# Kernel tuning notes

Hardware: AMD Instinct MI355X
Metric: run time of the kernel (lower is better)

## Reference

```python
import jax, jax.numpy as jnp
import numpy as np

N = 50000      # nodes
E = 640000     # edges
F_IN = 64      # node feature dim
H = 128        # hidden channels
G = 256        # graphs in batch
NEG_SLOPE = 0.2
BN_EPS = 1e-5


def setup_inputs() -> dict:
    key = jax.random.key(0)
    ks = jax.random.split(key, 32)
    rn = lambda k, shape, s=0.1: jax.random.normal(k, shape, dtype=jnp.float32) * s
    inp = {
        'x': jax.random.normal(ks[0], (N, F_IN), dtype=jnp.float32),
        'edge_index': jax.random.randint(ks[1], (2, E), 0, N, dtype=jnp.int32),
        'batch': jnp.sort(jax.random.randint(ks[2], (N,), 0, G, dtype=jnp.int32)),
        # GATConv 1
        'W1': rn(ks[3], (F_IN, H)), 'as1': rn(ks[4], (H,)), 'ad1': rn(ks[5], (H,)), 'b1': jnp.zeros((H,), jnp.float32),
        # GATConv 2
        'W2': rn(ks[6], (H, H)), 'as2': rn(ks[7], (H,)), 'ad2': rn(ks[8], (H,)), 'b2': jnp.zeros((H,), jnp.float32),
        # GATConv 3
        'W3': rn(ks[9], (H, H)), 'as3': rn(ks[10], (H,)), 'ad3': rn(ks[11], (H,)), 'b3': jnp.zeros((H,), jnp.float32),
        # BatchNorm (inference: running stats)
        'g1': jnp.ones((H,), jnp.float32), 'be1': jnp.zeros((H,), jnp.float32), 'm1': rn(ks[12], (H,), 0.01), 'v1': jnp.ones((H,), jnp.float32),
        'g2': jnp.ones((H,), jnp.float32), 'be2': jnp.zeros((H,), jnp.float32), 'm2': rn(ks[13], (H,), 0.01), 'v2': jnp.ones((H,), jnp.float32),
        'g3': jnp.ones((H,), jnp.float32), 'be3': jnp.zeros((H,), jnp.float32), 'm3': rn(ks[14], (H,), 0.01), 'v3': jnp.ones((H,), jnp.float32),
        # MLP head
        'lw1': rn(ks[15], (H, H)), 'lb1': jnp.zeros((H,), jnp.float32),
        'lw2': rn(ks[16], (H, 1)), 'lb2': jnp.zeros((1,), jnp.float32),
    }
    return inp


def gat_layer(x, src, dst, W, a_src, a_dst, b, n):
    # PyG GATConv, heads=1: linear, per-edge attention, segment softmax over dst, scatter-add.
    h = x @ W                                  # [N, H]
    s_src = h @ a_src                          # [N]
    s_dst = h @ a_dst                          # [N]
    e = jax.nn.leaky_relu(s_src[src] + s_dst[dst], NEG_SLOPE)   # [E']
    m = jax.ops.segment_max(e, dst, num_segments=n)
    ex = jnp.exp(e - m[dst])
    denom = jax.ops.segment_sum(ex, dst, num_segments=n)
    coef = ex / denom[dst]                     # softmax per destination node
    out = jax.ops.segment_sum(coef[:, None] * h[src], dst, num_segments=n)
    return out + b


def batch_norm(x, g, b, mean, var):
    return (x - mean) * jax.lax.rsqrt(var + BN_EPS) * g + b


def reference(x, edge_index, batch,
              W1, as1, ad1, b1, W2, as2, ad2, b2, W3, as3, ad3, b3,
              g1, be1, m1, v1, g2, be2, m2, v2, g3, be3, m3, v3,
              lw1, lb1, lw2, lb2):
    n = x.shape[0]
    loops = jnp.arange(n, dtype=edge_index.dtype)      # PyG adds self-loops by default
    src = jnp.concatenate([edge_index[0], loops])
    dst = jnp.concatenate([edge_index[1], loops])

    h = gat_layer(x, src, dst, W1, as1, ad1, b1, n)
    h = jax.nn.relu(batch_norm(h, g1, be1, m1, v1))
    h = gat_layer(h, src, dst, W2, as2, ad2, b2, n)
    h = jax.nn.relu(batch_norm(h, g2, be2, m2, v2))
    h = gat_layer(h, src, dst, W3, as3, ad3, b3, n)
    h = jax.nn.relu(batch_norm(h, g3, be3, m3, v3))

    # global_mean_pool
    counts = jax.ops.segment_sum(jnp.ones((n,), h.dtype), batch, num_segments=G)
    pooled = jax.ops.segment_sum(h, batch, num_segments=G) / jnp.maximum(counts, 1.0)[:, None]

    out = jax.nn.relu(pooled @ lw1 + lb1)
    out = out @ lw2 + lb2                               # [G, 1]
    return out
```

## Files before the change

### kernel.cpp

```cpp
#include <hip/hip_runtime.h>

#define HD 128
#define NEG 0.2f
#define BNEPS 1e-5f

typedef unsigned int uint32;
typedef __attribute__((ext_vector_type(8))) short short8;
typedef __attribute__((ext_vector_type(4))) float floatx4;


__device__ inline float wave_sum_f(float v) {
#pragma unroll
  for (int off = 32; off; off >>= 1) v += __shfl_xor(v, off, 64);
  return v;
}
__device__ inline int wave_iscan_i(int v, int lane) {
#pragma unroll
  for (int off = 1; off < 64; off <<= 1) {
    int t = __shfl_up(v, off, 64);
    if (lane >= off) v += t;
  }
  return v;
}
__device__ inline uint32 f2bf(float f) {
  uint32 u = __float_as_uint(f);
  return (u + 0x7fffu + ((u >> 16) & 1u)) >> 16;
}
__device__ inline void kpair(int kc, int lg, int e2, bool perm, int& k_lo, int& k_hi) {
  if (!perm) {
    k_lo = kc * 32 + lg * 8 + e2 * 2;
    k_hi = k_lo + 1;
  } else {
    int w = kc * 16 + lg * 4 + e2;
    k_lo = ((w >> 4) << 5) + (w & 15);
    k_hi = k_lo + 16;
  }
}

__global__ __launch_bounds__(256)
void k_pack(const float* __restrict__ W1, const float* __restrict__ as1v,
            const float* __restrict__ ad1v, const float* __restrict__ W2,
            const float* __restrict__ as2v, const float* __restrict__ ad2v,
            const float* __restrict__ W3, const float* __restrict__ as3v,
            const float* __restrict__ ad3v,
            const float* __restrict__ b1, const float* __restrict__ g1,
            const float* __restrict__ be1, const float* __restrict__ m1,
            const float* __restrict__ v1,
            const float* __restrict__ b2, const float* __restrict__ g2,
            const float* __restrict__ be2, const float* __restrict__ m2,
            const float* __restrict__ v2,
            const float* __restrict__ b3, const float* __restrict__ g3,
            const float* __restrict__ be3, const float* __restrict__ m3,
            const float* __restrict__ v3,
            uint32* __restrict__ PW1, uint32* __restrict__ PW2,
            uint32* __restrict__ PW3, uint32* __restrict__ BFA1,
            uint32* __restrict__ BFA2, uint32* __restrict__ BFA3,
            float4* __restrict__ BNAB, int* __restrict__ deg,
            int* __restrict__ gcnt, float* __restrict__ pooled, int G, int n) {
  const int b = blockIdx.x, t = threadIdx.x;
  if (b >= 83) {
    const int i = (b - 83) * 256 + t;
    if (i < n) deg[i] = 0;
    else if (i < n + G * HD) pooled[i - n] = 0.f;
    if (b == 83 && t == 0) gcnt[0] = 0;
    return;
  }
  if (b < 80) {
    const float* W;
    uint32* PW;
    int KC, local;
    bool perm;
    if (b < 16) { W = W1; PW = PW1; KC = 2; perm = false; local = b; }
    else if (b < 48) { W = W2; PW = PW2; KC = 4; perm = true; local = b - 16; }
    else { W = W3; PW = PW3; KC = 4; perm = true; local = b - 48; }
    const int idx = local * 256 + t;
    const int e2 = idx & 3, l = (idx >> 2) & 63, f = idx >> 8;
    const int kc = f % KC, ct = f / KC;
    int k_lo, k_hi;
    kpair(kc, l >> 4, e2, perm, k_lo, k_hi);
    const int col = ct * 16 + (l & 15);
    PW[idx] = f2bf(W[k_lo * HD + col]) | (f2bf(W[k_hi * HD + col]) << 16);
  } else {
    const int layer = b - 80;
    const float* W = layer == 0 ? W1 : layer == 1 ? W2 : W3;
    const float* av = layer == 0 ? as1v : layer == 1 ? as2v : as3v;
    const float* dv = layer == 0 ? ad1v : layer == 1 ? ad2v : ad3v;
    const float* bb = layer == 0 ? b1 : layer == 1 ? b2 : b3;
    const float* gg = layer == 0 ? g1 : layer == 1 ? g2 : g3;
    const float* bt = layer == 0 ? be1 : layer == 1 ? be2 : be3;
    const float* mm = layer == 0 ? m1 : layer == 1 ? m2 : m3;
    const float* vv = layer == 0 ? v1 : layer == 1 ? v2 : v3;
    uint32* BFA = layer == 0 ? BFA1 : layer == 1 ? BFA2 : BFA3;
    const int K = layer == 0 ? 64 : 128, KC = K / 32;
    const bool perm = layer != 0;
    __shared__ float ws[128], wd[128];
    if (t < K) {
      float s = 0.f, d = 0.f;
      for (int j = 0; j < HD; ++j) {
        const float w = W[t * HD + j];
        s = fmaf(w, av[j], s);
        d = fmaf(w, dv[j], d);
      }
      ws[t] = s;
      wd[t] = d;
    }
    __syncthreads();
    const int total = KC * 256;
    for (int idx = t; idx < total; idx += 256) {
      const int e2 = idx & 3, l = (idx >> 2) & 63, kc = idx >> 8;
      int k_lo, k_hi;
      kpair(kc, l >> 4, e2, perm, k_lo, k_hi);
      const int li = l & 15;
      const float lo = li == 0 ? ws[k_lo] : li == 1 ? wd[k_lo] : 0.f;
      const float hi = li == 0 ? ws[k_hi] : li == 1 ? wd[k_hi] : 0.f;
      BFA[idx] = f2bf(lo) | (f2bf(hi) << 16);
    }
    if (t < 64) {
      const int c0 = (t >> 4) * 32 + (t & 15);
      const int c1 = c0 + 16;
      const float A0 = gg[c0] * rsqrtf(vv[c0] + BNEPS);
      const float A1 = gg[c1] * rsqrtf(vv[c1] + BNEPS);
      float4 r;
      r.x = A0;
      r.y = (bb[c0] - mm[c0]) * A0 + bt[c0];
      r.z = A1;
      r.w = (bb[c1] - mm[c1]) * A1 + bt[c1];
      BNAB[layer * 64 + t] = r;
    }
  }
}

__global__ __launch_bounds__(256)
void k_alloc(const int* __restrict__ deg, int* __restrict__ gcnt,
             int2* __restrict__ offs2, int* __restrict__ csr,
             int* __restrict__ cursor, int n) {
  const int t = threadIdx.x, lane = t & 63, wave = t >> 6;
  const int i = blockIdx.x * 256 + t;
  const int v = (i < n) ? deg[i] + 1 : 0;
  const int x = wave_iscan_i(v, lane);
  __shared__ int wsum[4];
  __shared__ int bbase;
  if (lane == 63) wsum[wave] = x;
  __syncthreads();
  if (t == 0) bbase = atomicAdd(gcnt, wsum[0] + wsum[1] + wsum[2] + wsum[3]);
  __syncthreads();
  int add = bbase;
#pragma unroll
  for (int w = 0; w < 4; ++w)
    if (w < wave) add += wsum[w];
  const int start = add + x - v;
  if (i < n) {
    csr[start] = i;
    cursor[i] = start + 1;
    offs2[i] = make_int2(start, start + v);
  }
}

__global__ void k_fill_edges(const int* __restrict__ src, const int* __restrict__ dst,
                             int* __restrict__ cursor, int* __restrict__ csr, int E) {
  int i = blockIdx.x * blockDim.x + threadIdx.x;
  if (i < E) { int p = atomicAdd(&cursor[dst[i]], 1); csr[p] = src[i]; }
}

template <int K, bool BF16IN>
__device__ inline void gemm_body(int bid, const void* __restrict__ Xv,
                                 const uint32* __restrict__ PW,
                                 const uint32* __restrict__ BFA,
                                 uint32* __restrict__ Hh, float* __restrict__ ssrc,
                                 float* __restrict__ sdst, int n) {
  constexpr int KC = K / 32;
  __shared__ uint32 Xl[64 * K / 2];
  const int t = threadIdx.x;
  const int wv = t >> 6, l = t & 63;
  const int rowbase = bid * 64;

  short8 bfr[2][KC];
#pragma unroll
  for (int c2 = 0; c2 < 2; ++c2)
#pragma unroll
    for (int kc = 0; kc < KC; ++kc)
      bfr[c2][kc] = *((const short8*)PW + ((wv * 2 + c2) * KC + kc) * 64 + l);
  short8 bfa[KC];
  if (wv == 0) {
#pragma unroll
    for (int kc = 0; kc < KC; ++kc) bfa[kc] = *((const short8*)BFA + kc * 64 + l);
  }

  if (BF16IN) {
    const uint32* Xb = (const uint32*)Xv;
#pragma unroll
    for (int B = t; B < 64 * (K / 8); B += 256) {
      const int row = B / (K / 8), cb = B % (K / 8);
      const int r = min(rowbase + row, n - 1);
      const uint4 v = *(const uint4*)&Xb[(long)r * (K / 2) + cb * 4];
      *(uint4*)&Xl[row * (K / 2) + (cb ^ (row & 7)) * 4] = v;
    }
  } else {
    const float* X = (const float*)Xv;
    for (int i = t; i < 64 * (K / 4); i += 256) {
      const int row = i / (K / 4), kq = i % (K / 4);
      const int r = min(rowbase + row, n - 1);
      const float4 v = *(const float4*)&X[(long)r * K + kq * 4];
      uint2 p;
      p.x = f2bf(v.x) | (f2bf(v.y) << 16);
      p.y = f2bf(v.z) | (f2bf(v.w) << 16);
      int byte = row * (K * 2) + kq * 8;
      byte ^= (row & 7) << 4;
      *(uint2*)((char*)Xl + byte) = p;
    }
  }
  __syncthreads();

  floatx4 acc[4][2], acc2[4];
#pragma unroll
  for (int rt = 0; rt < 4; ++rt) {
    acc[rt][0] = (floatx4){0.f, 0.f, 0.f, 0.f};
    acc[rt][1] = (floatx4){0.f, 0.f, 0.f, 0.f};
    acc2[rt] = (floatx4){0.f, 0.f, 0.f, 0.f};
  }
  const int row_l = l & 15, kgrp = l >> 4;
#pragma unroll
  for (int rt = 0; rt < 4; ++rt) {
    const int row = rt * 16 + row_l;
#pragma unroll
    for (int kc = 0; kc < KC; ++kc) {
      const int byte = (row * (K * 2) + kc * 64 + kgrp * 16) ^ ((row & 7) << 4);
      const short8 af = *(const short8*)((const char*)Xl + byte);
      acc[rt][0] = __builtin_amdgcn_mfma_f32_16x16x32_bf16(af, bfr[0][kc], acc[rt][0], 0, 0, 0);
      acc[rt][1] = __builtin_amdgcn_mfma_f32_16x16x32_bf16(af, bfr[1][kc], acc[rt][1], 0, 0, 0);
      if (wv == 0)
        acc2[rt] = __builtin_amdgcn_mfma_f32_16x16x32_bf16(af, bfa[kc], acc2[rt], 0, 0, 0);
    }
  }

#pragma unroll
  for (int rt = 0; rt < 4; ++rt) {
#pragma unroll
    for (int r = 0; r < 4; ++r) {
      const int R = rowbase + rt * 16 + kgrp * 4 + r;
      if (R < n)
        Hh[(long)R * 64 + wv * 16 + row_l] =
            f2bf(acc[rt][0][r]) | (f2bf(acc[rt][1][r]) << 16);
    }
  }
  if (wv == 0 && row_l < 2) {
    float* tgt = (row_l == 0) ? ssrc : sdst;
#pragma unroll
    for (int rt = 0; rt < 4; ++rt)
#pragma unroll
      for (int r = 0; r < 4; ++r) {
        const int R = rowbase + rt * 16 + kgrp * 4 + r;
        if (R < n) tgt[R] = acc2[rt][r];
      }
  }
}

__global__ __launch_bounds__(256)
void k_gemm1_hist(const void* __restrict__ Xv, const uint32* __restrict__ PW,
                  const uint32* __restrict__ BFA, uint32* __restrict__ Hh,
                  float* __restrict__ ssrc, float* __restrict__ sdst, int n,
                  const int* __restrict__ dst, int* __restrict__ deg, int E, int GB) {
  const int b = blockIdx.x;
  if (b < GB) {
    gemm_body<64, false>(b, Xv, PW, BFA, Hh, ssrc, sdst, n);
  } else {
    const int i = (b - GB) * 256 + threadIdx.x;
    if (i < E) atomicAdd(&deg[dst[i]], 1);
  }
}

template <int K>
__global__ __launch_bounds__(256)
void k_gemm_mfma(const void* __restrict__ Xv, const uint32* __restrict__ PW,
                 const uint32* __restrict__ BFA, uint32* __restrict__ Hh,
                 float* __restrict__ ssrc, float* __restrict__ sdst, int n) {
  gemm_body<K, true>(blockIdx.x, Xv, PW, BFA, Hh, ssrc, sdst, n);
}

__global__ __launch_bounds__(256)
void k_agg(const uint32* __restrict__ Hh, const float* __restrict__ ssrc,
           const float* __restrict__ sdst, const int2* __restrict__ offs2,
           const int* __restrict__ csr, const float4* __restrict__ BNAB,
           uint32* __restrict__ Ybf, int n) {
  const int wid = (blockIdx.x * blockDim.x + threadIdx.x) >> 6;
  const int lane = threadIdx.x & 63;
  if (wid >= n) return;
  const int2 se = offs2[wid];
  const float sdv = sdst[wid];
  float acc0 = 0.f, acc1 = 0.f, denom = 0.f;
  for (int base = se.x; base < se.y; base += 64) {
    const int m = min(64, se.y - base);
    int sidx = 0;
    float p = 0.f;
    if (lane < m) {
      sidx = csr[base + lane];
      const float tt = ssrc[sidx] + sdv;
      const float e = (tt > 0.f) ? tt : NEG * tt;
      p = __expf(e);
    }
    denom += wave_sum_f(p);
    const uint32 pu = __float_as_uint(p);
    for (int jj = 0; jj < m; jj += 16) {
      uint32 g[16];
#pragma unroll
      for (int u = 0; u < 16; ++u) {
        if (jj + u < m) {
          const int s = __builtin_amdgcn_readlane(sidx, jj + u);
          g[u] = Hh[(long)s * 64 + lane];
        }
      }
#pragma unroll
      for (int u = 0; u < 16; ++u) {
        if (jj + u < m) {
          const float w = __uint_as_float(__builtin_amdgcn_readlane(pu, jj + u));
          acc0 = fmaf(w, __uint_as_float(g[u] << 16), acc0);
          acc1 = fmaf(w, __uint_as_float(g[u] & 0xffff0000u), acc1);
        }
      }
    }
  }
  const float inv = 1.f / denom;
  const float4 ab = BNAB[lane];
  const float v0 = fmaxf(fmaf(acc0 * inv, ab.x, ab.y), 0.f);
  const float v1 = fmaxf(fmaf(acc1 * inv, ab.z, ab.w), 0.f);
  Ybf[(long)wid * 64 + lane] = f2bf(v0) | (f2bf(v1) << 16);
}

__global__ __launch_bounds__(256)
void k_pool_part(const uint32* __restrict__ Ybf, const int* __restrict__ batch,
                 int n, float* __restrict__ pooled) {
  const int g = blockIdx.x >> 2, q = blockIdx.x & 3;
  const int wave = threadIdx.x >> 6, lane = threadIdx.x & 63;
  int lo = 0, hi = n;
  while (lo < hi) { int mid = (lo + hi) >> 1; if (batch[mid] < g) lo = mid + 1; else hi = mid; }
  const int start = lo;
  hi = n;
  while (lo < hi) { int mid = (lo + hi) >> 1; if (batch[mid] < g + 1) lo = mid + 1; else hi = mid; }
  const int len = lo - start;
  const int qs = start + (len * q) / 4;
  const int qe = start + (len * (q + 1)) / 4;
  const int c0 = (lane >> 4) * 32 + (lane & 15), c1 = c0 + 16;
  float m0 = 0.f, m1 = 0.f;
  for (int i = qs + wave; i < qe; i += 4) {
    const uint32 gv = Ybf[(long)i * 64 + lane];
    m0 += __uint_as_float(gv << 16);
    m1 += __uint_as_float(gv & 0xffff0000u);
  }
  __shared__ float red[4][HD];
  red[wave][c0] = m0;
  red[wave][c1] = m1;
  __syncthreads();
  if (wave == 0) {
    m0 = red[0][c0] + red[1][c0] + red[2][c0] + red[3][c0];
    m1 = red[0][c1] + red[1][c1] + red[2][c1] + red[3][c1];
    atomicAdd(&pooled[g * HD + c0], m0);
    atomicAdd(&pooled[g * HD + c1], m1);
  }
}

__global__ __launch_bounds__(256)
void k_head(const float* __restrict__ pooled, const int* __restrict__ batch, int n,
            int G, const float* __restrict__ lw1, const float* __restrict__ lb1,
            const float* __restrict__ lw2, const float* __restrict__ lb2,
            float* __restrict__ out) {
  const int g = blockIdx.x * 4 + (threadIdx.x >> 6);
  const int lane = threadIdx.x & 63;
  if (g >= G) return;
  int lo = 0, hi = n;
  while (lo < hi) { int mid = (lo + hi) >> 1; if (batch[mid] < g) lo = mid + 1; else hi = mid; }
  const int start = lo;
  hi = n;
  while (lo < hi) { int mid = (lo + hi) >> 1; if (batch[mid] < g + 1) lo = mid + 1; else hi = mid; }
  const int cnt = lo - start;
  const float invc = (cnt > 0) ? 1.f / (float)cnt : 0.f;
  const int c0 = (lane >> 4) * 32 + (lane & 15), c1 = c0 + 16;
  const float m0 = pooled[g * HD + c0] * invc;
  const float m1 = pooled[g * HD + c1] * invc;
  float t0 = lb1[c0], t1 = lb1[c1];
  for (int k = 0; k < HD; ++k) {
    const int srcl = ((k >> 5) << 4) + (k & 15);
    const float pv = __shfl(((k >> 4) & 1) ? m1 : m0, srcl, 64);
    t0 = fmaf(pv, lw1[k * HD + c0], t0);
    t1 = fmaf(pv, lw1[k * HD + c1], t1);
  }
  t0 = fmaxf(t0, 0.f);
  t1 = fmaxf(t1, 0.f);
  float p = t0 * lw2[c0] + t1 * lw2[c1];
#pragma unroll
  for (int off = 32; off; off >>= 1) p += __shfl_xor(p, off, 64);
  if (lane == 0) out[g] = p + lb2[0];
}


extern "C" void kernel_launch(void* const* d_in, const int* in_sizes, int n_in,
                              void* d_out, int out_size, void* d_ws, size_t ws_size,
                              hipStream_t stream) {
  const float* x = (const float*)d_in[0];
  const int* ei = (const int*)d_in[1];
  const int* batch = (const int*)d_in[2];
  const float* W1 = (const float*)d_in[3];
  const float* as1 = (const float*)d_in[4];
  const float* ad1 = (const float*)d_in[5];
  const float* b1 = (const float*)d_in[6];
  const float* W2 = (const float*)d_in[7];
  const float* as2 = (const float*)d_in[8];
  const float* ad2 = (const float*)d_in[9];
  const float* b2 = (const float*)d_in[10];
  const float* W3 = (const float*)d_in[11];
  const float* as3 = (const float*)d_in[12];
  const float* ad3 = (const float*)d_in[13];
  const float* b3 = (const float*)d_in[14];
  const float* g1 = (const float*)d_in[15];
  const float* be1 = (const float*)d_in[16];
  const float* m1 = (const float*)d_in[17];
  const float* v1 = (const float*)d_in[18];
  const float* g2 = (const float*)d_in[19];
  const float* be2 = (const float*)d_in[20];
  const float* m2 = (const float*)d_in[21];
  const float* v2 = (const float*)d_in[22];
  const float* g3 = (const float*)d_in[23];
  const float* be3 = (const float*)d_in[24];
  const float* m3 = (const float*)d_in[25];
  const float* v3 = (const float*)d_in[26];
  const float* lw1 = (const float*)d_in[27];
  const float* lb1 = (const float*)d_in[28];
  const float* lw2 = (const float*)d_in[29];
  const float* lb2 = (const float*)d_in[30];

  const int n = in_sizes[0] / 64;
  const int E = in_sizes[1] / 2;
  const int G = out_size;
  const int* src = ei;
  const int* dst = ei + E;

  uint32* hbuf = (uint32*)d_ws;
  uint32* ybuf = hbuf + (long)n * 64;
  float* ssrc = (float*)(ybuf + (long)n * 64);
  float* sdstv = ssrc + n;
  int* deg = (int*)(sdstv + n);
  int2* offs2 = (int2*)(deg + n);
  int* cursor = (int*)(offs2 + n);
  int* csr = cursor + n;
  int* gcnt = csr + (E + n);
  uint32* PW1 = (uint32*)(gcnt + 4);
  uint32* PW2 = PW1 + 4096;
  uint32* PW3 = PW2 + 8192;
  uint32* BFA1 = PW3 + 8192;
  uint32* BFA2 = BFA1 + 512;
  uint32* BFA3 = BFA2 + 1024;
  float4* BNAB = (float4*)(BFA3 + 1024);
  float* pooled = (float*)(BNAB + 3 * 64);

  const int B = 256;
  dim3 blk(B);
  const int nb = (n + B - 1) / B;
  const int eb = (E + B - 1) / B;
  const int zb = (n + G * HD + B - 1) / B;
  const int GB = (n + 63) / 64;

  k_pack<<<dim3(83 + zb), blk, 0, stream>>>(
      W1, as1, ad1, W2, as2, ad2, W3, as3, ad3,
      b1, g1, be1, m1, v1, b2, g2, be2, m2, v2, b3, g3, be3, m3, v3,
      PW1, PW2, PW3, BFA1, BFA2, BFA3, BNAB, deg, gcnt, pooled, G, n);
  k_gemm1_hist<<<dim3(GB + eb), blk, 0, stream>>>(x, PW1, BFA1, hbuf, ssrc, sdstv, n,
                                                  dst, deg, E, GB);
  k_alloc<<<dim3(nb), blk, 0, stream>>>(deg, gcnt, offs2, csr, cursor, n);
  k_fill_edges<<<dim3(eb), blk, 0, stream>>>(src, dst, cursor, csr, E);

  const dim3 agrid((n + 3) / 4);
  k_agg<<<agrid, blk, 0, stream>>>(hbuf, ssrc, sdstv, offs2, csr, BNAB + 0, ybuf, n);
  k_gemm_mfma<128><<<dim3(GB), blk, 0, stream>>>(ybuf, PW2, BFA2, hbuf, ssrc, sdstv, n);
  k_agg<<<agrid, blk, 0, stream>>>(hbuf, ssrc, sdstv, offs2, csr, BNAB + 64, ybuf, n);
  k_gemm_mfma<128><<<dim3(GB), blk, 0, stream>>>(ybuf, PW3, BFA3, hbuf, ssrc, sdstv, n);
  k_agg<<<agrid, blk, 0, stream>>>(hbuf, ssrc, sdstv, offs2, csr, BNAB + 128, ybuf, n);
  k_pool_part<<<dim3(4 * G), blk, 0, stream>>>(ybuf, batch, n, pooled);
  k_head<<<dim3((G + 3) / 4), blk, 0, stream>>>(pooled, batch, n, G, lw1, lb1, lw2,
                                                lb2, (float*)d_out);
}
```

Before: 225.9 us.

## Split aggregation into coefficient pass and column-sliced gather over sliced H layout

New measurement: 664.2 us. +194.0%, slower.

```diff
diff --git a/kernel.cpp b/kernel.cpp
--- a/kernel.cpp
+++ b/kernel.cpp
@@ -166,7 +166,7 @@
 __device__ inline void gemm_body(int bid, const void* __restrict__ Xv,
                                  const uint32* __restrict__ PW,
                                  const uint32* __restrict__ BFA,
-                                 uint32* __restrict__ Hh, float* __restrict__ ssrc,
+                                 uint32* __restrict__ SHh, float* __restrict__ ssrc,
                                  float* __restrict__ sdst, int n) {
   constexpr int KC = K / 32;
   __shared__ uint32 Xl[64 * K / 2];
@@ -233,13 +233,15 @@
     }
   }
 
+  const int w = wv * 16 + row_l;
+  const long slice_base = (long)(w >> 3) * n * 8 + (w & 7);
 #pragma unroll
   for (int rt = 0; rt < 4; ++rt) {
 #pragma unroll
     for (int r = 0; r < 4; ++r) {
       const int R = rowbase + rt * 16 + kgrp * 4 + r;
       if (R < n)
-        Hh[(long)R * 64 + wv * 16 + row_l] =
+        SHh[slice_base + (long)R * 8] =
             f2bf(acc[rt][0][r]) | (f2bf(acc[rt][1][r]) << 16);
     }
   }
@@ -257,12 +259,12 @@
 
 __global__ __launch_bounds__(256)
 void k_gemm1_hist(const void* __restrict__ Xv, const uint32* __restrict__ PW,
-                  const uint32* __restrict__ BFA, uint32* __restrict__ Hh,
+                  const uint32* __restrict__ BFA, uint32* __restrict__ SHh,
                   float* __restrict__ ssrc, float* __restrict__ sdst, int n,
                   const int* __restrict__ dst, int* __restrict__ deg, int E, int GB) {
   const int b = blockIdx.x;
   if (b < GB) {
-    gemm_body<64, false>(b, Xv, PW, BFA, Hh, ssrc, sdst, n);
+    gemm_body<64, false>(b, Xv, PW, BFA, SHh, ssrc, sdst, n);
   } else {
     const int i = (b - GB) * 256 + threadIdx.x;
     if (i < E) atomicAdd(&deg[dst[i]], 1);
@@ -272,58 +274,92 @@
 template <int K>
 __global__ __launch_bounds__(256)
 void k_gemm_mfma(const void* __restrict__ Xv, const uint32* __restrict__ PW,
-                 const uint32* __restrict__ BFA, uint32* __restrict__ Hh,
+                 const uint32* __restrict__ BFA, uint32* __restrict__ SHh,
                  float* __restrict__ ssrc, float* __restrict__ sdst, int n) {
-  gemm_body<K, true>(blockIdx.x, Xv, PW, BFA, Hh, ssrc, sdst, n);
-}
-
-__global__ __launch_bounds__(256)
-void k_agg(const uint32* __restrict__ Hh, const float* __restrict__ ssrc,
-           const float* __restrict__ sdst, const int2* __restrict__ offs2,
-           const int* __restrict__ csr, const float4* __restrict__ BNAB,
-           uint32* __restrict__ Ybf, int n) {
+  gemm_body<K, true>(blockIdx.x, Xv, PW, BFA, SHh, ssrc, sdst, n);
+}
+
+__global__ __launch_bounds__(256)
+void k_coef(const float* __restrict__ ssrc, const float* __restrict__ sdst,
+            const int2* __restrict__ offs2, const int* __restrict__ csr,
+            float* __restrict__ coef, int n) {
   const int wid = (blockIdx.x * blockDim.x + threadIdx.x) >> 6;
   const int lane = threadIdx.x & 63;
   if (wid >= n) return;
   const int2 se = offs2[wid];
   const float sdv = sdst[wid];
-  float acc0 = 0.f, acc1 = 0.f, denom = 0.f;
-  for (int base = se.x; base < se.y; base += 64) {
-    const int m = min(64, se.y - base);
-    int sidx = 0;
+  const int len = se.y - se.x;
+  if (len <= 64) {
     float p = 0.f;
-    if (lane < m) {
-      sidx = csr[base + lane];
-      const float tt = ssrc[sidx] + sdv;
+    if (lane < len) {
+      const int s = csr[se.x + lane];
+      const float tt = ssrc[s] + sdv;
       const float e = (tt > 0.f) ? tt : NEG * tt;
       p = __expf(e);
     }
-    denom += wave_sum_f(p);
-    const uint32 pu = __float_as_uint(p);
-    for (int jj = 0; jj < m; jj += 16) {
-      uint32 g[16];
-#pragma unroll
-      for (int u = 0; u < 16; ++u) {
-        if (jj + u < m) {
-          const int s = __builtin_amdgcn_readlane(sidx, jj + u);
-          g[u] = Hh[(long)s * 64 + lane];
-        }
+    const float inv = 1.f / wave_sum_f(p);
+    if (lane < len) coef[se.x + lane] = p * inv;
+  } else {
+    float denom = 0.f;
+    for (int base = se.x; base < se.y; base += 64) {
+      const int m = min(64, se.y - base);
+      float p = 0.f;
+      if (lane < m) {
+        const int s = csr[base + lane];
+        const float tt = ssrc[s] + sdv;
+        const float e = (tt > 0.f) ? tt : NEG * tt;
+        p = __expf(e);
       }
-#pragma unroll
-      for (int u = 0; u < 16; ++u) {
-        if (jj + u < m) {
-          const float w = __uint_as_float(__builtin_amdgcn_readlane(pu, jj + u));
-          acc0 = fmaf(w, __uint_as_float(g[u] << 16), acc0);
-          acc1 = fmaf(w, __uint_as_float(g[u] & 0xffff0000u), acc1);
-        }
+      denom += wave_sum_f(p);
+    }
+    const float inv = 1.f / denom;
+    for (int base = se.x; base < se.y; base += 64) {
+      const int m = min(64, se.y - base);
+      if (lane < m) {
+        const int s = csr[base + lane];
+        const float tt = ssrc[s] + sdv;
+        const float e = (tt > 0.f) ? tt : NEG * tt;
+        coef[base + lane] = __expf(e) * inv;
       }
     }
   }
-  const float inv = 1.f / denom;
-  const float4 ab = BNAB[lane];
-  const float v0 = fmaxf(fmaf(acc0 * inv, ab.x, ab.y), 0.f);
-  const float v1 = fmaxf(fmaf(acc1 * inv, ab.z, ab.w), 0.f);
-  Ybf[(long)wid * 64 + lane] = f2bf(v0) | (f2bf(v1) << 16);
+}
+
+__global__ __launch_bounds__(256)
+void k_slice(const uint32* __restrict__ SHh, const float* __restrict__ coef,
+             const int2* __restrict__ offs2, const int* __restrict__ csr,
+             const float4* __restrict__ BNAB, uint32* __restrict__ Ybf, int n) {
+  const int k = blockIdx.x & 7;
+  const int node0 = (blockIdx.x >> 3) * 64 + (threadIdx.x >> 6) * 16;
+  const int lane = threadIdx.x & 63;
+  const int eg = lane >> 3, wd = lane & 7;
+  const uint32* T = SHh + (long)k * n * 8;
+  const float4 ab = BNAB[k * 8 + wd];
+  for (int u = 0; u < 16; ++u) {
+    const int node = node0 + u;
+    if (node >= n) return;
+    const int2 se = offs2[node];
+    float a0 = 0.f, a1 = 0.f;
+    for (int j = se.x + eg; j < se.y; j += 8) {
+      const int s = __builtin_nontemporal_load(&csr[j]);
+      const float c = __builtin_nontemporal_load(&coef[j]);
+      const uint32 g = T[(long)s * 8 + wd];
+      a0 = fmaf(c, __uint_as_float(g << 16), a0);
+      a1 = fmaf(c, __uint_as_float(g & 0xffff0000u), a1);
+    }
+    a0 += __shfl_xor(a0, 8, 64);
+    a1 += __shfl_xor(a1, 8, 64);
+    a0 += __shfl_xor(a0, 16, 64);
+    a1 += __shfl_xor(a1, 16, 64);
+    a0 += __shfl_xor(a0, 32, 64);
+    a1 += __shfl_xor(a1, 32, 64);
+    if (eg == 0) {
+      const float v0 = fmaxf(fmaf(a0, ab.x, ab.y), 0.f);
+      const float v1 = fmaxf(fmaf(a1, ab.z, ab.w), 0.f);
+      __builtin_nontemporal_store(f2bf(v0) | (f2bf(v1) << 16),
+                                  &Ybf[(long)node * 64 + k * 8 + wd]);
+    }
+  }
 }
 
 __global__ __launch_bounds__(256)
@@ -441,7 +477,8 @@
   int2* offs2 = (int2*)(deg + n);
   int* cursor = (int*)(offs2 + n);
   int* csr = cursor + n;
-  int* gcnt = csr + (E + n);
+  float* coef = (float*)(csr + (E + n));
+  int* gcnt = (int*)(coef + (E + n));
   uint32* PW1 = (uint32*)(gcnt + 4);
   uint32* PW2 = PW1 + 4096;
   uint32* PW3 = PW2 + 8192;
@@ -467,12 +504,16 @@
   k_alloc<<<dim3(nb), blk, 0, stream>>>(deg, gcnt, offs2, csr, cursor, n);
   k_fill_edges<<<dim3(eb), blk, 0, stream>>>(src, dst, cursor, csr, E);
 
-  const dim3 agrid((n + 3) / 4);
-  k_agg<<<agrid, blk, 0, stream>>>(hbuf, ssrc, sdstv, offs2, csr, BNAB + 0, ybuf, n);
+  const dim3 cgrid((n + 3) / 4);
+  const dim3 sgrid(8 * GB);
+  k_coef<<<cgrid, blk, 0, stream>>>(ssrc, sdstv, offs2, csr, coef, n);
+  k_slice<<<sgrid, blk, 0, stream>>>(hbuf, coef, offs2, csr, BNAB + 0, ybuf, n);
   k_gemm_mfma<128><<<dim3(GB), blk, 0, stream>>>(ybuf, PW2, BFA2, hbuf, ssrc, sdstv, n);
-  k_agg<<<agrid, blk, 0, stream>>>(hbuf, ssrc, sdstv, offs2, csr, BNAB + 64, ybuf, n);
+  k_coef<<<cgrid, blk, 0, stream>>>(ssrc, sdstv, offs2, csr, coef, n);
+  k_slice<<<sgrid, blk, 0, stream>>>(hbuf, coef, offs2, csr, BNAB + 64, ybuf, n);
   k_gemm_mfma<128><<<dim3(GB), blk, 0, stream>>>(ybuf, PW3, BFA3, hbuf, ssrc, sdstv, n);
-  k_agg<<<agrid, blk, 0, stream>>>(hbuf, ssrc, sdstv, offs2, csr, BNAB + 128, ybuf, n);
+  k_coef<<<cgrid, blk, 0, stream>>>(ssrc, sdstv, offs2, csr, coef, n);
+  k_slice<<<sgrid, blk, 0, stream>>>(hbuf, coef, offs2, csr, BNAB + 128, ybuf, n);
   k_pool_part<<<dim3(4 * G), blk, 0, stream>>>(ybuf, batch, n, pooled);
   k_head<<<dim3((G + 3) / 4), blk, 0, stream>>>(pooled, batch, n, G, lw1, lb1, lw2,
                                                 lb2, (float*)d_out);
```
